# Performance work log

Measured on AMD Instinct MI355X. Metric: run time of the kernel, lower is better.

The kernel has to match this reference:

```python
import jax, jax.numpy as jnp
import numpy as np

G = 100000   # num graphs
N = 2000000  # num nodes
E = 4000000  # num edges (unused downstream, kept for fidelity)
D = 300      # emb_dim
L = 50       # num noise levels


def setup_inputs() -> dict:
    key = jax.random.key(0)
    ks = jax.random.split(key, 12)
    node2graph = jnp.sort(jax.random.randint(ks[0], (N,), 0, G))
    edge_index = jax.random.randint(ks[1], (2, E), 0, N)
    noise_level = jax.random.randint(ks[2], (G,), 0, L)
    molecule_repr = jax.random.normal(ks[3], (G, D), dtype=jnp.float32)
    pos_noise_pred = jax.random.normal(ks[4], (N, 3), dtype=jnp.float32)
    pos_perturbed = jax.random.normal(ks[5], (N, 3), dtype=jnp.float32)
    pos_target = jax.random.normal(ks[6], (N, 3), dtype=jnp.float32)
    s = 1.0 / np.sqrt(D)
    W1 = jax.random.uniform(ks[7], (D, D), minval=-s, maxval=s, dtype=jnp.float32)
    b1 = jax.random.uniform(ks[8], (D,), minval=-s, maxval=s, dtype=jnp.float32)
    W2 = jax.random.uniform(ks[9], (D, D), minval=-s, maxval=s, dtype=jnp.float32)
    b2 = jax.random.uniform(ks[10], (D,), minval=-s, maxval=s, dtype=jnp.float32)
    sigmas = jnp.asarray(np.exp(np.linspace(np.log(10.0), np.log(0.01), L)), dtype=jnp.float32)
    return dict(node2graph=node2graph, edge_index=edge_index, noise_level=noise_level,
                num_graphs=G, molecule_repr=molecule_repr, pos_noise_pred=pos_noise_pred,
                pos_perturbed=pos_perturbed, pos_target=pos_target,
                W1=W1, b1=b1, W2=W2, b2=b2, sigmas=sigmas)


def _score_target_riemann(pos_perturbed, pos_target, node2graph, num_graphs):
    # @torch.no_grad() branch: all scatter_mean/scatter_add indexed by node2graph
    seg_sum = lambda x: jax.ops.segment_sum(x, node2graph, num_segments=num_graphs)
    cnt = jnp.maximum(seg_sum(jnp.ones((node2graph.shape[0],), jnp.float32)), 1.0)[:, None]
    center = seg_sum(pos_target) / cnt                 # [G,3]
    p_center = seg_sum(pos_perturbed) / cnt            # [G,3]
    pos_c = pos_target - center[node2graph]            # [N,3]
    pp_c = pos_perturbed - p_center[node2graph]        # [N,3]
    # per-graph 3x3 matrices: ptp[i,j] = sum pp_i*pp_j, otp[i,j] = sum pos_c_i*pp_j
    ptp = seg_sum(pp_c[:, :, None] * pp_c[:, None, :])   # [G,3,3]
    otp = seg_sum(pos_c[:, :, None] * pp_c[:, None, :])  # [G,3,3]
    ptp_n = ptp[node2graph]                              # [N,3,3]
    otp_n = otp[node2graph]                              # [N,3,3]
    num = -2.0 * (jnp.einsum('ni,nij->nj', pp_c, ptp_n)
                  - jnp.einsum('ni,nij->nj', pos_c, otp_n))  # [N,3]
    den = (jnp.linalg.norm(ptp_n.reshape(-1, 9), axis=-1)
           + jnp.linalg.norm(otp_n.reshape(-1, 9), axis=-1))[:, None]
    return num / den


def reference(node2graph, edge_index, noise_level, num_graphs, molecule_repr,
              pos_noise_pred, pos_perturbed, pos_target, W1, b1, W2, b2, sigmas):
    edge2graph = node2graph[edge_index[0]]  # computed but unused, as in original
    used_sigmas = sigmas[noise_level][node2graph][:, None]  # [N,1]
    score_target = jax.lax.stop_gradient(
        _score_target_riemann(pos_perturbed, pos_target, node2graph, num_graphs)
    ) / used_sigmas
    pred_noise = (pos_noise_pred - pos_perturbed) * (1.0 / used_sigmas)
    per_node = jnp.sum((pred_noise - score_target) ** 2, axis=-1)  # [N]
    per_graph = jax.ops.segment_sum(per_node, node2graph, num_segments=num_graphs)
    pos_denoise = per_graph.mean()
    # noise-level prediction head: Linear -> SiLU -> Linear, CE over noise_level
    h = jax.nn.silu(molecule_repr @ W1 + b1)
    logits = h @ W2 + b2  # [G,D]
    logp = jax.nn.log_softmax(logits, axis=-1)
    ce = -jnp.take_along_axis(logp, noise_level[:, None], axis=1)[:, 0]
    loss_pred_noise = ce.mean()
    return jnp.stack([pos_denoise, loss_pred_noise])
```

## Files before the change

kernel.cpp:

```cpp
#include <hip/hip_runtime.h>
#include <math.h>


typedef __attribute__((ext_vector_type(8))) short bf16x8;
typedef __attribute__((ext_vector_type(4))) short s16x4;
typedef __attribute__((ext_vector_type(4))) float f32x4;

__device__ __forceinline__ short bt(float f) {
    return (short)(__float_as_uint(f) >> 16);
}

#define TM   32
#define DRL  300
#define DP   320
#define XS   328
#define NT   20
#define NW   5
#define KCH  10


__global__ __launch_bounds__(256)
void k_bnd(const int* __restrict__ n2g, int* __restrict__ gs,
           int* __restrict__ ge, int N) {
    int t = blockIdx.x * blockDim.x + threadIdx.x;
    if (t >= N) return;
    int g = n2g[t];
    if (t == 0     || n2g[t - 1] != g) gs[g] = t;
    if (t == N - 1 || n2g[t + 1] != g) ge[g] = t + 1;
}

__global__ __launch_bounds__(256)
void k_graph(const int* __restrict__ gs, const int* __restrict__ ge,
             const float* __restrict__ pt, const float* __restrict__ pp,
             const float* __restrict__ pnp,
             const int* __restrict__ nl, const float* __restrict__ sigmas,
             double* __restrict__ accA, int G) {
    const int tg = blockIdx.x * blockDim.x + threadIdx.x;
    const int g  = tg >> 2;
    const int j  = tg & 3;
    float q = 0.f;
    if (g < G) {
        const int s = gs[g], e = ge[g];
        const int g0 = s >> 2, g1 = (e + 3) >> 2;
        const float4* ptv = (const float4*)pt;
        const float4* ppv = (const float4*)pp;
        const float4* pnv = (const float4*)pnp;
        float st0=0,st1=0,st2=0, sp0=0,sp1=0,sp2=0;
        float m00=0,m01=0,m02=0,m11=0,m12=0,m22=0;
        float t00=0,t01=0,t02=0,t10=0,t11=0,t12=0,t20=0,t21=0,t22=0;
        for (int gg = g0 + j; gg < g1; gg += 4) {
            float4 x0 = ptv[3*gg], x1 = ptv[3*gg+1], x2 = ptv[3*gg+2];
            float4 y0 = ppv[3*gg], y1 = ppv[3*gg+1], y2 = ppv[3*gg+2];
            float A[12] = {x0.x,x0.y,x0.z,x0.w, x1.x,x1.y,x1.z,x1.w,
                           x2.x,x2.y,x2.z,x2.w};
            float B[12] = {y0.x,y0.y,y0.z,y0.w, y1.x,y1.y,y1.z,y1.w,
                           y2.x,y2.y,y2.z,y2.w};
            const int base = gg * 4;
#pragma unroll
            for (int k = 0; k < 4; ++k) {
                const int i = base + k;
                const bool v = (i >= s) && (i < e);
                float a0 = v ? A[3*k+0] : 0.f;
                float a1 = v ? A[3*k+1] : 0.f;
                float a2 = v ? A[3*k+2] : 0.f;
                float b0 = v ? B[3*k+0] : 0.f;
                float b1 = v ? B[3*k+1] : 0.f;
                float b2 = v ? B[3*k+2] : 0.f;
                st0 += a0; st1 += a1; st2 += a2;
                sp0 += b0; sp1 += b1; sp2 += b2;
                m00 += b0*b0; m01 += b0*b1; m02 += b0*b2;
                m11 += b1*b1; m12 += b1*b2; m22 += b2*b2;
                t00 += a0*b0; t01 += a0*b1; t02 += a0*b2;
                t10 += a1*b0; t11 += a1*b1; t12 += a1*b2;
                t20 += a2*b0; t21 += a2*b1; t22 += a2*b2;
            }
        }
#define QR(x) do { x += __shfl_xor(x, 1, 64); x += __shfl_xor(x, 2, 64); } while (0)
        QR(st0); QR(st1); QR(st2); QR(sp0); QR(sp1); QR(sp2);
        QR(m00); QR(m01); QR(m02); QR(m11); QR(m12); QR(m22);
        QR(t00); QR(t01); QR(t02); QR(t10); QR(t11); QR(t12);
        QR(t20); QR(t21); QR(t22);
#undef QR
        float cnt = fmaxf((float)(e - s), 1.f);
        float ic  = 1.f / cnt;
        float c0 = st0 * ic, c1 = st1 * ic, c2 = st2 * ic;
        float d0 = sp0 * ic, d1 = sp1 * ic, d2 = sp2 * ic;
        float p00 = m00 - cnt*d0*d0, p01 = m01 - cnt*d0*d1;
        float p02 = m02 - cnt*d0*d2, p11 = m11 - cnt*d1*d1;
        float p12 = m12 - cnt*d1*d2, p22 = m22 - cnt*d2*d2;
        float o00 = t00 - cnt*c0*d0, o01 = t01 - cnt*c0*d1, o02 = t02 - cnt*c0*d2;
        float o10 = t10 - cnt*c1*d0, o11 = t11 - cnt*c1*d1, o12 = t12 - cnt*c1*d2;
        float o20 = t20 - cnt*c2*d0, o21 = t21 - cnt*c2*d1, o22 = t22 - cnt*c2*d2;
        float ptn = sqrtf(p00*p00 + p11*p11 + p22*p22 +
                          2.f*(p01*p01 + p02*p02 + p12*p12));
        float otn = sqrtf(o00*o00 + o01*o01 + o02*o02 +
                          o10*o10 + o11*o11 + o12*o12 +
                          o20*o20 + o21*o21 + o22*o22);
        float den = ptn + otn;
        float idn = (den > 0.f) ? (1.f / den) : 0.f;
        float sg  = sigmas[nl[g]];
        float is2 = 1.f / (sg * sg);
        for (int gg = g0 + j; gg < g1; gg += 4) {
            float4 x0 = ptv[3*gg], x1 = ptv[3*gg+1], x2 = ptv[3*gg+2];
            float4 y0 = ppv[3*gg], y1 = ppv[3*gg+1], y2 = ppv[3*gg+2];
            float4 z0 = pnv[3*gg], z1 = pnv[3*gg+1], z2 = pnv[3*gg+2];
            float A[12] = {x0.x,x0.y,x0.z,x0.w, x1.x,x1.y,x1.z,x1.w,
                           x2.x,x2.y,x2.z,x2.w};
            float B[12] = {y0.x,y0.y,y0.z,y0.w, y1.x,y1.y,y1.z,y1.w,
                           y2.x,y2.y,y2.z,y2.w};
            float C[12] = {z0.x,z0.y,z0.z,z0.w, z1.x,z1.y,z1.z,z1.w,
                           z2.x,z2.y,z2.z,z2.w};
            const int base = gg * 4;
#pragma unroll
            for (int k = 0; k < 4; ++k) {
                const int i = base + k;
                const bool v = (i >= s) && (i < e);
                float a0 = A[3*k+0] - c0, a1 = A[3*k+1] - c1, a2 = A[3*k+2] - c2;
                float bb0 = B[3*k+0], bb1 = B[3*k+1], bb2 = B[3*k+2];
                float b0 = bb0 - d0, b1 = bb1 - d1, b2 = bb2 - d2;
                float n0 = -2.f * ((b0*p00 + b1*p01 + b2*p02) - (a0*o00 + a1*o10 + a2*o20));
                float n1 = -2.f * ((b0*p01 + b1*p11 + b2*p12) - (a0*o01 + a1*o11 + a2*o21));
                float n2 = -2.f * ((b0*p02 + b1*p12 + b2*p22) - (a0*o02 + a1*o12 + a2*o22));
                float e0 = (C[3*k+0] - bb0) - n0 * idn;
                float e1 = (C[3*k+1] - bb1) - n1 * idn;
                float e2 = (C[3*k+2] - bb2) - n2 * idn;
                float contrib = (e0*e0 + e1*e1 + e2*e2) * is2;
                q += v ? contrib : 0.f;
            }
        }
    }
    for (int o = 32; o > 0; o >>= 1) q += __shfl_down(q, o, 64);
    if ((threadIdx.x & 63) == 0)
        atomicAdd(&accA[(blockIdx.x * 4 + (threadIdx.x >> 6)) & 255], (double)q);
}


__global__ void k_prepw(const float* __restrict__ W1, const float* __restrict__ W2,
                        short* __restrict__ Wb1, short* __restrict__ Wb2) {
    int id = blockIdx.x * blockDim.x + threadIdx.x;
    if (id >= 2 * DP * DP) return;
    int mat = id / (DP * DP);
    int rem = id - mat * DP * DP;
    int k = rem / DP, n = rem - (rem / DP) * DP;
    const float* W = mat ? W2 : W1;
    short* Wb = mat ? Wb2 : Wb1;
    float v = (k < DRL && n < DRL) ? W[k * DRL + n] : 0.f;
    int kc = k >> 5, kin = k & 31, quad = kin >> 3, j = kin & 7;
    int t = n >> 4, l16 = n & 15;
    Wb[(((kc * NT + t) * 64) + quad * 16 + l16) * 8 + j] = bt(v);
}


__global__ __launch_bounds__(256, 4)
void k_mlp(const float* __restrict__ X,
           const short* __restrict__ Wb1, const short* __restrict__ Wb2,
           const float* __restrict__ b1, const float* __restrict__ b2,
           const int* __restrict__ nl,
           double* __restrict__ accC, int G) {
    __shared__ __align__(16) short Xs[TM * XS];

    const int tid  = threadIdx.x;
    const int wv   = tid >> 6;
    const int lane = tid & 63;
    const int quad = lane >> 4;
    const int l16  = lane & 15;
    const int m0   = blockIdx.x * TM;
    const int tb0  = wv * NW;

    const float4* Xv = (const float4*)X;
    for (int idx = tid; idx < TM * 75; idx += 256) {
        int r = idx / 75, c = idx - r * 75;
        int gr = m0 + r;
        float4 v = {0.f, 0.f, 0.f, 0.f};
        if (gr < G) v = Xv[gr * 75 + c];
        s16x4 sv = { bt(v.x), bt(v.y), bt(v.z), bt(v.w) };
        *(s16x4*)&Xs[r * XS + c * 4] = sv;
    }
    for (int idx = tid; idx < TM * (DP - DRL); idx += 256) {
        int r = idx / (DP - DRL), c = idx - r * (DP - DRL);
        Xs[r * XS + DRL + c] = 0;
    }
    __syncthreads();

    const bf16x8* B1 = (const bf16x8*)Wb1;
    const bf16x8* B2 = (const bf16x8*)Wb2;

    f32x4 acc[2][NW];
    const f32x4 vzero = {0.f, 0.f, 0.f, 0.f};
#pragma unroll
    for (int m = 0; m < 2; ++m)
#pragma unroll
        for (int n = 0; n < NW; ++n) acc[m][n] = vzero;

    {
        bf16x8 nb[NW];
#pragma unroll
        for (int n = 0; n < NW; ++n) nb[n] = B1[(0 * NT + tb0 + n) * 64 + lane];
#pragma unroll
        for (int kc = 0; kc < KCH; ++kc) {
            bf16x8 bv[NW];
#pragma unroll
            for (int n = 0; n < NW; ++n) bv[n] = nb[n];
            if (kc + 1 < KCH) {
#pragma unroll
                for (int n = 0; n < NW; ++n)
                    nb[n] = B1[((kc + 1) * NT + tb0 + n) * 64 + lane];
            }
            bf16x8 a0 = *(const bf16x8*)&Xs[(l16) * XS + kc * 32 + quad * 8];
            bf16x8 a1 = *(const bf16x8*)&Xs[(16 + l16) * XS + kc * 32 + quad * 8];
#pragma unroll
            for (int n = 0; n < NW; ++n) {
                acc[0][n] = __builtin_amdgcn_mfma_f32_16x16x32_bf16(a0, bv[n], acc[0][n], 0, 0, 0);
                acc[1][n] = __builtin_amdgcn_mfma_f32_16x16x32_bf16(a1, bv[n], acc[1][n], 0, 0, 0);
            }
        }
    }
    __syncthreads();

#pragma unroll
    for (int n = 0; n < NW; ++n) {
        int col = (tb0 + n) * 16 + l16;
        float bias = (col < DRL) ? b1[col] : 0.f;
#pragma unroll
        for (int m = 0; m < 2; ++m)
#pragma unroll
            for (int r = 0; r < 4; ++r) {
                float v = acc[m][n][r] + bias;
                float h = v / (1.f + __expf(-v));
                Xs[(m * 16 + quad * 4 + r) * XS + col] = bt(h);
            }
    }
    __syncthreads();

#pragma unroll
    for (int m = 0; m < 2; ++m)
#pragma unroll
        for (int n = 0; n < NW; ++n) acc[m][n] = vzero;
    {
        bf16x8 nb[NW];
#pragma unroll
        for (int n = 0; n < NW; ++n) nb[n] = B2[(0 * NT + tb0 + n) * 64 + lane];
#pragma unroll
        for (int kc = 0; kc < KCH; ++kc) {
            bf16x8 bv[NW];
#pragma unroll
            for (int n = 0; n < NW; ++n) bv[n] = nb[n];
            if (kc + 1 < KCH) {
#pragma unroll
                for (int n = 0; n < NW; ++n)
                    nb[n] = B2[((kc + 1) * NT + tb0 + n) * 64 + lane];
            }
            bf16x8 a0 = *(const bf16x8*)&Xs[(l16) * XS + kc * 32 + quad * 8];
            bf16x8 a1 = *(const bf16x8*)&Xs[(16 + l16) * XS + kc * 32 + quad * 8];
#pragma unroll
            for (int n = 0; n < NW; ++n) {
                acc[0][n] = __builtin_amdgcn_mfma_f32_16x16x32_bf16(a0, bv[n], acc[0][n], 0, 0, 0);
                acc[1][n] = __builtin_amdgcn_mfma_f32_16x16x32_bf16(a1, bv[n], acc[1][n], 0, 0, 0);
            }
        }
    }
    __syncthreads();

    float* S = (float*)Xs;
    float* T = S + TM * 4;
#pragma unroll
    for (int m = 0; m < 2; ++m) {
#pragma unroll
        for (int r = 0; r < 4; ++r) {
            int row = m * 16 + quad * 4 + r;
            int grow = m0 + row;
            int ct = (grow < G) ? nl[grow] : -1;
            float sw = 0.f;
#pragma unroll
            for (int n = 0; n < NW; ++n) {
                int col = (tb0 + n) * 16 + l16;
                float lg = acc[m][n][r] + ((col < DRL) ? b2[col] : 0.f);
                if (col < DRL) sw += __expf(lg);
                if (col == ct) T[row] = lg;
            }
            for (int o = 1; o < 16; o <<= 1) sw += __shfl_xor(sw, o, 64);
            if (l16 == 0) S[row * 4 + wv] = sw;
        }
    }
    __syncthreads();
    if (tid < 64) {
        float q = 0.f;
        int row = tid;
        if (row < TM) {
            int grow = m0 + row;
            if (grow < G) {
                float ss = S[row*4+0] + S[row*4+1] + S[row*4+2] + S[row*4+3];
                q = __logf(ss) - T[row];
            }
        }
        for (int o = 32; o > 0; o >>= 1) q += __shfl_down(q, o, 64);
        if (tid == 0) atomicAdd(&accC[blockIdx.x & 255], (double)q);
    }
}


__global__ void k_final(const double* __restrict__ accA,
                        const double* __restrict__ accC,
                        float* __restrict__ out, float invG) {
    int t = threadIdx.x;
    double a = accA[t] + accA[t + 64] + accA[t + 128] + accA[t + 192];
    double c = accC[t] + accC[t + 64] + accC[t + 128] + accC[t + 192];
    for (int o = 32; o > 0; o >>= 1) {
        a += __shfl_down(a, o, 64);
        c += __shfl_down(c, o, 64);
    }
    if (t == 0) {
        out[0] = (float)(a * (double)invG);
        out[1] = (float)(c * (double)invG);
    }
}


extern "C" void kernel_launch(void* const* d_in, const int* in_sizes, int n_in,
                              void* d_out, int out_size, void* d_ws, size_t ws_size,
                              hipStream_t stream) {
    const int*   n2g = (const int*)d_in[0];
    const int*   nl  = (const int*)d_in[2];
    const float* X   = (const float*)d_in[4];
    const float* pnp = (const float*)d_in[5];
    const float* pp  = (const float*)d_in[6];
    const float* pt  = (const float*)d_in[7];
    const float* W1  = (const float*)d_in[8];
    const float* b1  = (const float*)d_in[9];
    const float* W2  = (const float*)d_in[10];
    const float* b2  = (const float*)d_in[11];
    const float* sig = (const float*)d_in[12];

    const int N = in_sizes[0];
    const int G = in_sizes[2];

    double* accA = (double*)d_ws;
    double* accC = accA + 256;
    short*  Wb1  = (short*)((char*)d_ws + 4096);
    short*  Wb2  = Wb1 + DP * DP;
    int*    gs   = (int*)((char*)d_ws + 4096 + (size_t)2 * DP * DP * 2);
    int*    ge   = gs + G;

    hipMemsetAsync(d_ws, 0, 4096, stream);
    hipMemsetAsync(gs, 0, (size_t)2 * G * 4, stream);

    k_prepw<<<(2 * DP * DP + 255) / 256, 256, 0, stream>>>(W1, W2, Wb1, Wb2);
    k_bnd<<<(N + 255) / 256, 256, 0, stream>>>(n2g, gs, ge, N);
    k_graph<<<(4 * G + 255) / 256, 256, 0, stream>>>(gs, ge, pt, pp, pnp,
                                                     nl, sig, accA, G);
    k_mlp<<<(G + TM - 1) / TM, 256, 0, stream>>>(X, Wb1, Wb2, b1, b2, nl,
                                                 accC, G);
    k_final<<<1, 64, 0, stream>>>(accA, accC, (float*)d_out, 1.0f / (float)G);
}
```

Measured before the change: 380.7 us.

## Fuse prep kernels and interleave graph-loss and MLP blocks in one launch

Merges the weight-conversion and boundary-detection kernels into one launch, and merges the per-graph loss kernel with the MLP/cross-entropy kernel into a single grid where every third block does graph work and the other two do MLP tiles. This removes launch gaps and lets the memory-bound graph blocks overlap with the MFMA-bound MLP blocks on the same CUs. It also drops the register prefetch of weight fragments in the MLP k-loops. The fused kernel carries the MLP's shared memory and launch bounds for graph blocks too, which may limit their occupancy.

```diff
diff --git a/kernel.cpp b/kernel.cpp
--- a/kernel.cpp
+++ b/kernel.cpp
@@ -19,152 +19,161 @@
 #define KCH  10
 
 
+#define NB_PREPW 800
+
 __global__ __launch_bounds__(256)
-void k_bnd(const int* __restrict__ n2g, int* __restrict__ gs,
-           int* __restrict__ ge, int N) {
-    int t = blockIdx.x * blockDim.x + threadIdx.x;
-    if (t >= N) return;
-    int g = n2g[t];
-    if (t == 0     || n2g[t - 1] != g) gs[g] = t;
-    if (t == N - 1 || n2g[t + 1] != g) ge[g] = t + 1;
-}
-
-__global__ __launch_bounds__(256)
-void k_graph(const int* __restrict__ gs, const int* __restrict__ ge,
-             const float* __restrict__ pt, const float* __restrict__ pp,
-             const float* __restrict__ pnp,
-             const int* __restrict__ nl, const float* __restrict__ sigmas,
-             double* __restrict__ accA, int G) {
-    const int tg = blockIdx.x * blockDim.x + threadIdx.x;
-    const int g  = tg >> 2;
-    const int j  = tg & 3;
-    float q = 0.f;
-    if (g < G) {
-        const int s = gs[g], e = ge[g];
-        const int g0 = s >> 2, g1 = (e + 3) >> 2;
-        const float4* ptv = (const float4*)pt;
-        const float4* ppv = (const float4*)pp;
-        const float4* pnv = (const float4*)pnp;
-        float st0=0,st1=0,st2=0, sp0=0,sp1=0,sp2=0;
-        float m00=0,m01=0,m02=0,m11=0,m12=0,m22=0;
-        float t00=0,t01=0,t02=0,t10=0,t11=0,t12=0,t20=0,t21=0,t22=0;
-        for (int gg = g0 + j; gg < g1; gg += 4) {
-            float4 x0 = ptv[3*gg], x1 = ptv[3*gg+1], x2 = ptv[3*gg+2];
-            float4 y0 = ppv[3*gg], y1 = ppv[3*gg+1], y2 = ppv[3*gg+2];
-            float A[12] = {x0.x,x0.y,x0.z,x0.w, x1.x,x1.y,x1.z,x1.w,
-                           x2.x,x2.y,x2.z,x2.w};
-            float B[12] = {y0.x,y0.y,y0.z,y0.w, y1.x,y1.y,y1.z,y1.w,
-                           y2.x,y2.y,y2.z,y2.w};
-            const int base = gg * 4;
-#pragma unroll
-            for (int k = 0; k < 4; ++k) {
-                const int i = base + k;
-                const bool v = (i >= s) && (i < e);
-                float a0 = v ? A[3*k+0] : 0.f;
-                float a1 = v ? A[3*k+1] : 0.f;
-                float a2 = v ? A[3*k+2] : 0.f;
-                float b0 = v ? B[3*k+0] : 0.f;
-                float b1 = v ? B[3*k+1] : 0.f;
-                float b2 = v ? B[3*k+2] : 0.f;
-                st0 += a0; st1 += a1; st2 += a2;
-                sp0 += b0; sp1 += b1; sp2 += b2;
-                m00 += b0*b0; m01 += b0*b1; m02 += b0*b2;
-                m11 += b1*b1; m12 += b1*b2; m22 += b2*b2;
-                t00 += a0*b0; t01 += a0*b1; t02 += a0*b2;
-                t10 += a1*b0; t11 += a1*b1; t12 += a1*b2;
-                t20 += a2*b0; t21 += a2*b1; t22 += a2*b2;
-            }
-        }
+void k_prep(const float* __restrict__ W1, const float* __restrict__ W2,
+            short* __restrict__ Wb1, short* __restrict__ Wb2,
+            const int* __restrict__ n2g, int* __restrict__ gs,
+            int* __restrict__ ge, int N) {
+    const int bid = blockIdx.x;
+    const int tid = threadIdx.x;
+    if (bid < NB_PREPW) {
+        int id = bid * 256 + tid;
+        int mat = id / (DP * DP);
+        int rem = id - mat * DP * DP;
+        int k = rem / DP, n = rem - (rem / DP) * DP;
+        const float* W = mat ? W2 : W1;
+        short* Wb = mat ? Wb2 : Wb1;
+        float v = (k < DRL && n < DRL) ? W[k * DRL + n] : 0.f;
+        int kc = k >> 5, kin = k & 31, quad = kin >> 3, j = kin & 7;
+        int t = n >> 4, l16 = n & 15;
+        Wb[(((kc * NT + t) * 64) + quad * 16 + l16) * 8 + j] = bt(v);
+    } else {
+        int t = (bid - NB_PREPW) * 256 + tid;
+        if (t < N) {
+            int g = n2g[t];
+            if (t == 0     || n2g[t - 1] != g) gs[g] = t;
+            if (t == N - 1 || n2g[t + 1] != g) ge[g] = t + 1;
+        }
+    }
+}
+
+
+__global__ __launch_bounds__(256, 4)
+void k_main(const int* __restrict__ gs, const int* __restrict__ ge,
+            const float* __restrict__ pt, const float* __restrict__ pp,
+            const float* __restrict__ pnp,
+            const int* __restrict__ nl, const float* __restrict__ sigmas,
+            double* __restrict__ accA,
+            const float* __restrict__ X,
+            const short* __restrict__ Wb1, const short* __restrict__ Wb2,
+            const float* __restrict__ b1, const float* __restrict__ b2,
+            double* __restrict__ accC, int G) {
+    __shared__ __align__(16) short Xs[TM * XS];
+
+    const int bid = blockIdx.x;
+    const int tid = threadIdx.x;
+    const int t3  = bid / 3;
+    const int r3  = bid - t3 * 3;
+
+    if (r3 == 0) {
+        const int tg = t3 * 256 + tid;
+        const int g  = tg >> 2;
+        const int j  = tg & 3;
+        float q = 0.f;
+        if (g < G) {
+            const int s = gs[g], e = ge[g];
+            const int g0 = s >> 2, g1 = (e + 3) >> 2;
+            const float4* ptv = (const float4*)pt;
+            const float4* ppv = (const float4*)pp;
+            const float4* pnv = (const float4*)pnp;
+            float st0=0,st1=0,st2=0, sp0=0,sp1=0,sp2=0;
+            float m00=0,m01=0,m02=0,m11=0,m12=0,m22=0;
+            float t00=0,t01=0,t02=0,t10=0,t11=0,t12=0,t20=0,t21=0,t22=0;
+            for (int gg = g0 + j; gg < g1; gg += 4) {
+                float4 x0 = ptv[3*gg], x1 = ptv[3*gg+1], x2 = ptv[3*gg+2];
+                float4 y0 = ppv[3*gg], y1 = ppv[3*gg+1], y2 = ppv[3*gg+2];
+                float A[12] = {x0.x,x0.y,x0.z,x0.w, x1.x,x1.y,x1.z,x1.w,
+                               x2.x,x2.y,x2.z,x2.w};
+                float B[12] = {y0.x,y0.y,y0.z,y0.w, y1.x,y1.y,y1.z,y1.w,
+                               y2.x,y2.y,y2.z,y2.w};
+                const int base = gg * 4;
+#pragma unroll
+                for (int k = 0; k < 4; ++k) {
+                    const int i = base + k;
+                    const bool v = (i >= s) && (i < e);
+                    float a0 = v ? A[3*k+0] : 0.f;
+                    float a1 = v ? A[3*k+1] : 0.f;
+                    float a2 = v ? A[3*k+2] : 0.f;
+                    float b0 = v ? B[3*k+0] : 0.f;
+                    float b1v = v ? B[3*k+1] : 0.f;
+                    float b2v = v ? B[3*k+2] : 0.f;
+                    st0 += a0; st1 += a1; st2 += a2;
+                    sp0 += b0; sp1 += b1v; sp2 += b2v;
+                    m00 += b0*b0;  m01 += b0*b1v;  m02 += b0*b2v;
+                    m11 += b1v*b1v; m12 += b1v*b2v; m22 += b2v*b2v;
+                    t00 += a0*b0; t01 += a0*b1v; t02 += a0*b2v;
+                    t10 += a1*b0; t11 += a1*b1v; t12 += a1*b2v;
+                    t20 += a2*b0; t21 += a2*b1v; t22 += a2*b2v;
+                }
+            }
 #define QR(x) do { x += __shfl_xor(x, 1, 64); x += __shfl_xor(x, 2, 64); } while (0)
-        QR(st0); QR(st1); QR(st2); QR(sp0); QR(sp1); QR(sp2);
-        QR(m00); QR(m01); QR(m02); QR(m11); QR(m12); QR(m22);
-        QR(t00); QR(t01); QR(t02); QR(t10); QR(t11); QR(t12);
-        QR(t20); QR(t21); QR(t22);
+            QR(st0); QR(st1); QR(st2); QR(sp0); QR(sp1); QR(sp2);
+            QR(m00); QR(m01); QR(m02); QR(m11); QR(m12); QR(m22);
+            QR(t00); QR(t01); QR(t02); QR(t10); QR(t11); QR(t12);
+            QR(t20); QR(t21); QR(t22);
 #undef QR
-        float cnt = fmaxf((float)(e - s), 1.f);
-        float ic  = 1.f / cnt;
-        float c0 = st0 * ic, c1 = st1 * ic, c2 = st2 * ic;
-        float d0 = sp0 * ic, d1 = sp1 * ic, d2 = sp2 * ic;
-        float p00 = m00 - cnt*d0*d0, p01 = m01 - cnt*d0*d1;
-        float p02 = m02 - cnt*d0*d2, p11 = m11 - cnt*d1*d1;
-        float p12 = m12 - cnt*d1*d2, p22 = m22 - cnt*d2*d2;
-        float o00 = t00 - cnt*c0*d0, o01 = t01 - cnt*c0*d1, o02 = t02 - cnt*c0*d2;
-        float o10 = t10 - cnt*c1*d0, o11 = t11 - cnt*c1*d1, o12 = t12 - cnt*c1*d2;
-        float o20 = t20 - cnt*c2*d0, o21 = t21 - cnt*c2*d1, o22 = t22 - cnt*c2*d2;
-        float ptn = sqrtf(p00*p00 + p11*p11 + p22*p22 +
-                          2.f*(p01*p01 + p02*p02 + p12*p12));
-        float otn = sqrtf(o00*o00 + o01*o01 + o02*o02 +
-                          o10*o10 + o11*o11 + o12*o12 +
-                          o20*o20 + o21*o21 + o22*o22);
-        float den = ptn + otn;
-        float idn = (den > 0.f) ? (1.f / den) : 0.f;
-        float sg  = sigmas[nl[g]];
-        float is2 = 1.f / (sg * sg);
-        for (int gg = g0 + j; gg < g1; gg += 4) {
-            float4 x0 = ptv[3*gg], x1 = ptv[3*gg+1], x2 = ptv[3*gg+2];
-            float4 y0 = ppv[3*gg], y1 = ppv[3*gg+1], y2 = ppv[3*gg+2];
-            float4 z0 = pnv[3*gg], z1 = pnv[3*gg+1], z2 = pnv[3*gg+2];
-            float A[12] = {x0.x,x0.y,x0.z,x0.w, x1.x,x1.y,x1.z,x1.w,
-                           x2.x,x2.y,x2.z,x2.w};
-            float B[12] = {y0.x,y0.y,y0.z,y0.w, y1.x,y1.y,y1.z,y1.w,
-                           y2.x,y2.y,y2.z,y2.w};
-            float C[12] = {z0.x,z0.y,z0.z,z0.w, z1.x,z1.y,z1.z,z1.w,
-                           z2.x,z2.y,z2.z,z2.w};
-            const int base = gg * 4;
-#pragma unroll
-            for (int k = 0; k < 4; ++k) {
-                const int i = base + k;
-                const bool v = (i >= s) && (i < e);
-                float a0 = A[3*k+0] - c0, a1 = A[3*k+1] - c1, a2 = A[3*k+2] - c2;
-                float bb0 = B[3*k+0], bb1 = B[3*k+1], bb2 = B[3*k+2];
-                float b0 = bb0 - d0, b1 = bb1 - d1, b2 = bb2 - d2;
-                float n0 = -2.f * ((b0*p00 + b1*p01 + b2*p02) - (a0*o00 + a1*o10 + a2*o20));
-                float n1 = -2.f * ((b0*p01 + b1*p11 + b2*p12) - (a0*o01 + a1*o11 + a2*o21));
-                float n2 = -2.f * ((b0*p02 + b1*p12 + b2*p22) - (a0*o02 + a1*o12 + a2*o22));
-                float e0 = (C[3*k+0] - bb0) - n0 * idn;
-                float e1 = (C[3*k+1] - bb1) - n1 * idn;
-                float e2 = (C[3*k+2] - bb2) - n2 * idn;
-                float contrib = (e0*e0 + e1*e1 + e2*e2) * is2;
-                q += v ? contrib : 0.f;
-            }
-        }
-    }
-    for (int o = 32; o > 0; o >>= 1) q += __shfl_down(q, o, 64);
-    if ((threadIdx.x & 63) == 0)
-        atomicAdd(&accA[(blockIdx.x * 4 + (threadIdx.x >> 6)) & 255], (double)q);
-}
-
-
-__global__ void k_prepw(const float* __restrict__ W1, const float* __restrict__ W2,
-                        short* __restrict__ Wb1, short* __restrict__ Wb2) {
-    int id = blockIdx.x * blockDim.x + threadIdx.x;
-    if (id >= 2 * DP * DP) return;
-    int mat = id / (DP * DP);
-    int rem = id - mat * DP * DP;
-    int k = rem / DP, n = rem - (rem / DP) * DP;
-    const float* W = mat ? W2 : W1;
-    short* Wb = mat ? Wb2 : Wb1;
-    float v = (k < DRL && n < DRL) ? W[k * DRL + n] : 0.f;
-    int kc = k >> 5, kin = k & 31, quad = kin >> 3, j = kin & 7;
-    int t = n >> 4, l16 = n & 15;
-    Wb[(((kc * NT + t) * 64) + quad * 16 + l16) * 8 + j] = bt(v);
-}
-
-
-__global__ __launch_bounds__(256, 4)
-void k_mlp(const float* __restrict__ X,
-           const short* __restrict__ Wb1, const short* __restrict__ Wb2,
-           const float* __restrict__ b1, const float* __restrict__ b2,
-           const int* __restrict__ nl,
-           double* __restrict__ accC, int G) {
-    __shared__ __align__(16) short Xs[TM * XS];
-
-    const int tid  = threadIdx.x;
+            float cnt = fmaxf((float)(e - s), 1.f);
+            float ic  = 1.f / cnt;
+            float c0 = st0 * ic, c1 = st1 * ic, c2 = st2 * ic;
+            float d0 = sp0 * ic, d1 = sp1 * ic, d2 = sp2 * ic;
+            float p00 = m00 - cnt*d0*d0, p01 = m01 - cnt*d0*d1;
+            float p02 = m02 - cnt*d0*d2, p11 = m11 - cnt*d1*d1;
+            float p12 = m12 - cnt*d1*d2, p22 = m22 - cnt*d2*d2;
+            float o00 = t00 - cnt*c0*d0, o01 = t01 - cnt*c0*d1, o02 = t02 - cnt*c0*d2;
+            float o10 = t10 - cnt*c1*d0, o11 = t11 - cnt*c1*d1, o12 = t12 - cnt*c1*d2;
+            float o20 = t20 - cnt*c2*d0, o21 = t21 - cnt*c2*d1, o22 = t22 - cnt*c2*d2;
+            float ptn = sqrtf(p00*p00 + p11*p11 + p22*p22 +
+                              2.f*(p01*p01 + p02*p02 + p12*p12));
+            float otn = sqrtf(o00*o00 + o01*o01 + o02*o02 +
+                              o10*o10 + o11*o11 + o12*o12 +
+                              o20*o20 + o21*o21 + o22*o22);
+            float den = ptn + otn;
+            float idn = (den > 0.f) ? (1.f / den) : 0.f;
+            float sg  = sigmas[nl[g]];
+            float is2 = 1.f / (sg * sg);
+            for (int gg = g0 + j; gg < g1; gg += 4) {
+                float4 x0 = ptv[3*gg], x1 = ptv[3*gg+1], x2 = ptv[3*gg+2];
+                float4 y0 = ppv[3*gg], y1 = ppv[3*gg+1], y2 = ppv[3*gg+2];
+                float4 z0 = pnv[3*gg], z1 = pnv[3*gg+1], z2 = pnv[3*gg+2];
+                float A[12] = {x0.x,x0.y,x0.z,x0.w, x1.x,x1.y,x1.z,x1.w,
+                               x2.x,x2.y,x2.z,x2.w};
+                float B[12] = {y0.x,y0.y,y0.z,y0.w, y1.x,y1.y,y1.z,y1.w,
+                               y2.x,y2.y,y2.z,y2.w};
+                float C[12] = {z0.x,z0.y,z0.z,z0.w, z1.x,z1.y,z1.z,z1.w,
+                               z2.x,z2.y,z2.z,z2.w};
+                const int base = gg * 4;
+#pragma unroll
+                for (int k = 0; k < 4; ++k) {
+                    const int i = base + k;
+                    const bool v = (i >= s) && (i < e);
+                    float a0 = A[3*k+0] - c0, a1 = A[3*k+1] - c1, a2 = A[3*k+2] - c2;
+                    float bb0 = B[3*k+0], bb1 = B[3*k+1], bb2 = B[3*k+2];
+                    float b0 = bb0 - d0, b1v = bb1 - d1, b2v = bb2 - d2;
+                    float n0 = -2.f * ((b0*p00 + b1v*p01 + b2v*p02) - (a0*o00 + a1*o10 + a2*o20));
+                    float n1 = -2.f * ((b0*p01 + b1v*p11 + b2v*p12) - (a0*o01 + a1*o11 + a2*o21));
+                    float n2 = -2.f * ((b0*p02 + b1v*p12 + b2v*p22) - (a0*o02 + a1*o12 + a2*o22));
+                    float e0 = (C[3*k+0] - bb0) - n0 * idn;
+                    float e1 = (C[3*k+1] - bb1) - n1 * idn;
+                    float e2 = (C[3*k+2] - bb2) - n2 * idn;
+                    float contrib = (e0*e0 + e1*e1 + e2*e2) * is2;
+                    q += v ? contrib : 0.f;
+                }
+            }
+        }
+        for (int o = 32; o > 0; o >>= 1) q += __shfl_down(q, o, 64);
+        if ((tid & 63) == 0)
+            atomicAdd(&accA[(t3 * 4 + (tid >> 6)) & 255], (double)q);
+        return;
+    }
+
+    const int mid = t3 * 2 + (r3 - 1);
     const int wv   = tid >> 6;
     const int lane = tid & 63;
     const int quad = lane >> 4;
     const int l16  = lane & 15;
-    const int m0   = blockIdx.x * TM;
+    const int m0   = mid * TM;
     const int tb0  = wv * NW;
 
     const float4* Xv = (const float4*)X;
@@ -192,27 +201,17 @@
 #pragma unroll
         for (int n = 0; n < NW; ++n) acc[m][n] = vzero;
 
-    {
-        bf16x8 nb[NW];
-#pragma unroll
-        for (int n = 0; n < NW; ++n) nb[n] = B1[(0 * NT + tb0 + n) * 64 + lane];
-#pragma unroll
-        for (int kc = 0; kc < KCH; ++kc) {
-            bf16x8 bv[NW];
-#pragma unroll
-            for (int n = 0; n < NW; ++n) bv[n] = nb[n];
-            if (kc + 1 < KCH) {
-#pragma unroll
-                for (int n = 0; n < NW; ++n)
-                    nb[n] = B1[((kc + 1) * NT + tb0 + n) * 64 + lane];
-            }
-            bf16x8 a0 = *(const bf16x8*)&Xs[(l16) * XS + kc * 32 + quad * 8];
-            bf16x8 a1 = *(const bf16x8*)&Xs[(16 + l16) * XS + kc * 32 + quad * 8];
-#pragma unroll
-            for (int n = 0; n < NW; ++n) {
-                acc[0][n] = __builtin_amdgcn_mfma_f32_16x16x32_bf16(a0, bv[n], acc[0][n], 0, 0, 0);
-                acc[1][n] = __builtin_amdgcn_mfma_f32_16x16x32_bf16(a1, bv[n], acc[1][n], 0, 0, 0);
-            }
+#pragma unroll
+    for (int kc = 0; kc < KCH; ++kc) {
+        bf16x8 bv[NW];
+#pragma unroll
+        for (int n = 0; n < NW; ++n) bv[n] = B1[(kc * NT + tb0 + n) * 64 + lane];
+        bf16x8 a0 = *(const bf16x8*)&Xs[(l16) * XS + kc * 32 + quad * 8];
+        bf16x8 a1 = *(const bf16x8*)&Xs[(16 + l16) * XS + kc * 32 + quad * 8];
+#pragma unroll
+        for (int n = 0; n < NW; ++n) {
+            acc[0][n] = __builtin_amdgcn_mfma_f32_16x16x32_bf16(a0, bv[n], acc[0][n], 0, 0, 0);
+            acc[1][n] = __builtin_amdgcn_mfma_f32_16x16x32_bf16(a1, bv[n], acc[1][n], 0, 0, 0);
         }
     }
     __syncthreads();
@@ -236,27 +235,17 @@
     for (int m = 0; m < 2; ++m)
 #pragma unroll
         for (int n = 0; n < NW; ++n) acc[m][n] = vzero;
-    {
-        bf16x8 nb[NW];
-#pragma unroll
-        for (int n = 0; n < NW; ++n) nb[n] = B2[(0 * NT + tb0 + n) * 64 + lane];
-#pragma unroll
-        for (int kc = 0; kc < KCH; ++kc) {
-            bf16x8 bv[NW];
-#pragma unroll
-            for (int n = 0; n < NW; ++n) bv[n] = nb[n];
-            if (kc + 1 < KCH) {
-#pragma unroll
-                for (int n = 0; n < NW; ++n)
-                    nb[n] = B2[((kc + 1) * NT + tb0 + n) * 64 + lane];
-            }
-            bf16x8 a0 = *(const bf16x8*)&Xs[(l16) * XS + kc * 32 + quad * 8];
-            bf16x8 a1 = *(const bf16x8*)&Xs[(16 + l16) * XS + kc * 32 + quad * 8];
-#pragma unroll
-            for (int n = 0; n < NW; ++n) {
-                acc[0][n] = __builtin_amdgcn_mfma_f32_16x16x32_bf16(a0, bv[n], acc[0][n], 0, 0, 0);
-                acc[1][n] = __builtin_amdgcn_mfma_f32_16x16x32_bf16(a1, bv[n], acc[1][n], 0, 0, 0);
-            }
+#pragma unroll
+    for (int kc = 0; kc < KCH; ++kc) {
+        bf16x8 bv[NW];
+#pragma unroll
+        for (int n = 0; n < NW; ++n) bv[n] = B2[(kc * NT + tb0 + n) * 64 + lane];
+        bf16x8 a0 = *(const bf16x8*)&Xs[(l16) * XS + kc * 32 + quad * 8];
+        bf16x8 a1 = *(const bf16x8*)&Xs[(16 + l16) * XS + kc * 32 + quad * 8];
+#pragma unroll
+        for (int n = 0; n < NW; ++n) {
+            acc[0][n] = __builtin_amdgcn_mfma_f32_16x16x32_bf16(a0, bv[n], acc[0][n], 0, 0, 0);
+            acc[1][n] = __builtin_amdgcn_mfma_f32_16x16x32_bf16(a1, bv[n], acc[1][n], 0, 0, 0);
         }
     }
     __syncthreads();
@@ -294,7 +283,7 @@
             }
         }
         for (int o = 32; o > 0; o >>= 1) q += __shfl_down(q, o, 64);
-        if (tid == 0) atomicAdd(&accC[blockIdx.x & 255], (double)q);
+        if (tid == 0) atomicAdd(&accC[mid & 255], (double)q);
     }
 }
 
@@ -344,11 +333,13 @@
     hipMemsetAsync(d_ws, 0, 4096, stream);
     hipMemsetAsync(gs, 0, (size_t)2 * G * 4, stream);
 
-    k_prepw<<<(2 * DP * DP + 255) / 256, 256, 0, stream>>>(W1, W2, Wb1, Wb2);
-    k_bnd<<<(N + 255) / 256, 256, 0, stream>>>(n2g, gs, ge, N);
-    k_graph<<<(4 * G + 255) / 256, 256, 0, stream>>>(gs, ge, pt, pp, pnp,
-                                                     nl, sig, accA, G);
-    k_mlp<<<(G + TM - 1) / TM, 256, 0, stream>>>(X, Wb1, Wb2, b1, b2, nl,
-                                                 accC, G);
+    const int nb_bnd = (N + 255) / 256;
+    const int nbg    = (4 * G + 255) / 256;
+    const int nmain  = 3 * nbg;
+
+    k_prep<<<NB_PREPW + nb_bnd, 256, 0, stream>>>(W1, W2, Wb1, Wb2,
+                                                  n2g, gs, ge, N);
+    k_main<<<nmain, 256, 0, stream>>>(gs, ge, pt, pp, pnp, nl, sig, accA,
+                                      X, Wb1, Wb2, b1, b2, accC, G);
     k_final<<<1, 64, 0, stream>>>(accA, accC, (float*)d_out, 1.0f / (float)G);
 }
```

After: 358.7 us. 1.06x faster.
